# Kernel tuning notes

Measured on AMD Instinct MI355X. Metric: run time of the kernel, lower is better.

The kernel has to match this reference:

```python
import jax, jax.numpy as jnp
import numpy as np

N = 100000      # nodes
E = 3200000     # edges
IN_DIM = 128
HID = 128
OUT_DIM = 1
LAYERS = 8
ALPHA = 0.1
THETA = 0.5


def setup_inputs() -> dict:
    key = jax.random.key(0)
    ks = jax.random.split(key, 8)
    x = jax.random.normal(ks[0], (N, IN_DIM), dtype=jnp.float32)
    edge_index = jax.random.randint(ks[1], (2, E), 0, N, dtype=jnp.int64)
    edge_weight = jax.random.uniform(ks[2], (E,), dtype=jnp.float32)  # unused by original forward path
    W_in = jax.random.normal(ks[3], (IN_DIM, HID), dtype=jnp.float32) * 0.05
    b_in = jnp.zeros((HID,), dtype=jnp.float32)
    W_gcn = jax.random.normal(ks[4], (LAYERS, HID, HID), dtype=jnp.float32) * 0.05
    W_out = jax.random.normal(ks[5], (HID, OUT_DIM), dtype=jnp.float32) * 0.05
    b_out = jnp.zeros((OUT_DIM,), dtype=jnp.float32)
    return {"x": x, "edge_weight": edge_weight, "W_in": W_in, "b_in": b_in,
            "W_gcn": W_gcn, "W_out": W_out, "b_out": b_out, "edge_index": edge_index}


def _gcn_norm(edge_index, dtype):
    # add self loops (fill value 1), symmetric normalization deg^-1/2 A deg^-1/2
    sl = jnp.arange(N, dtype=edge_index.dtype)
    row = jnp.concatenate([edge_index[0], sl])
    col = jnp.concatenate([edge_index[1], sl])
    w = jnp.ones(row.shape[0], dtype=dtype)
    deg = jax.ops.segment_sum(w, col, num_segments=N)
    dinv = jnp.where(deg > 0, jax.lax.rsqrt(deg), 0.0)
    norm = dinv[row] * dinv[col]
    return row, col, norm


def reference(x, edge_weight, W_in, b_in, W_gcn, W_out, b_out, edge_index):
    row, col, norm = _gcn_norm(edge_index, x.dtype)
    h = x @ W_in + b_in            # initial_proj
    h0 = h                          # residual x0
    for i in range(LAYERS):
        # dropout is identity in eval mode
        msg = h[row] * norm[:, None]                       # gather + scale [E+N, HID]
        agg = jax.ops.segment_sum(msg, col, num_segments=N)
        s = (1.0 - ALPHA) * agg + ALPHA * h0               # identity-mapped residual
        beta = float(np.log(THETA / (i + 1) + 1.0))
        h = (1.0 - beta) * s + beta * (s @ W_gcn[i])       # GCNII weight mix
        h = jax.nn.relu(h)
    return h @ W_out + b_out
```

## Files before the change

### kernel.cpp

```cpp
#include <hip/hip_runtime.h>
#include <hip/hip_bf16.h>
#include <math.h>

#define N_NODES 100000
#define N_EDGES 3200000
#define HID 128
#define LAYERS 8
#define ALPHA 0.1f
#define THETA 0.5f

#define SCAN_TILE 1024
#define NB_SCAN ((N_NODES + SCAN_TILE - 1) / SCAN_TILE)

typedef unsigned int uint;
typedef unsigned short ushort;
typedef __attribute__((ext_vector_type(8))) short short8;
typedef __attribute__((ext_vector_type(4))) float f32x4;

__device__ inline float bf_lo(uint p) { return __uint_as_float(p << 16); }
__device__ inline float bf_hi(uint p) { return __uint_as_float(p & 0xffff0000u); }
__device__ inline uint bf_pack(float x, float y) {
    uint ux = __float_as_uint(x), uy = __float_as_uint(y);
    uint rx = (ux + 0x7fffu + ((ux >> 16) & 1u)) >> 16;
    uint ry = (uy + 0x7fffu + ((uy >> 16) & 1u)) >> 16;
    return rx | (ry << 16);
}
__device__ inline ushort bfr(float x) {
    uint u = __float_as_uint(x);
    return (ushort)((u + 0x7fffu + ((u >> 16) & 1u)) >> 16);
}
__device__ inline float bff(ushort s) { return __uint_as_float(((uint)s) << 16); }

__global__ __launch_bounds__(256) void k_count(const int* __restrict__ col,
                                               int* __restrict__ cnt) {
    int e = blockIdx.x * 256 + threadIdx.x;
    if (e < N_EDGES) atomicAdd(&cnt[col[e]], 1);
}

__global__ __launch_bounds__(256) void k_dinv(const int* __restrict__ cnt,
                                              float* __restrict__ dinv) {
    int n = blockIdx.x * 256 + threadIdx.x;
    if (n < N_NODES) dinv[n] = rsqrtf((float)(cnt[n] + 1));
}

__global__ __launch_bounds__(256) void k_scan1(const int* __restrict__ cnt,
                                               int* __restrict__ indptr,
                                               int* __restrict__ bsum) {
    __shared__ int lds[256];
    int t = threadIdx.x;
    int base = blockIdx.x * SCAN_TILE + t * 4;
    int v[4];
    int s = 0;
#pragma unroll
    for (int j = 0; j < 4; ++j) {
        v[j] = (base + j < N_NODES) ? cnt[base + j] : 0;
        s += v[j];
    }
    lds[t] = s;
    __syncthreads();
    for (int off = 1; off < 256; off <<= 1) {
        int u = (t >= off) ? lds[t - off] : 0;
        __syncthreads();
        lds[t] += u;
        __syncthreads();
    }
    int run = lds[t] - s;
#pragma unroll
    for (int j = 0; j < 4; ++j) {
        if (base + j < N_NODES) indptr[base + j] = run;
        run += v[j];
    }
    if (t == 255) bsum[blockIdx.x] = lds[255];
}

__global__ __launch_bounds__(256) void k_scan2(const int* __restrict__ bsum,
                                               int* __restrict__ boff) {
    __shared__ int lds[256];
    int t = threadIdx.x;
    int v = (t < NB_SCAN) ? bsum[t] : 0;
    lds[t] = v;
    __syncthreads();
    for (int off = 1; off < 256; off <<= 1) {
        int u = (t >= off) ? lds[t - off] : 0;
        __syncthreads();
        lds[t] += u;
        __syncthreads();
    }
    boff[t] = lds[t] - v;
}

__global__ __launch_bounds__(256) void k_scan3(int* __restrict__ indptr,
                                               const int* __restrict__ boff) {
    int base = blockIdx.x * SCAN_TILE + threadIdx.x * 4;
    int add = boff[blockIdx.x];
#pragma unroll
    for (int j = 0; j < 4; ++j) {
        if (base + j < N_NODES) indptr[base + j] += add;
    }
    if (blockIdx.x == 0 && threadIdx.x == 0) indptr[N_NODES] = N_EDGES;
}

__global__ __launch_bounds__(256) void k_fill(const int* __restrict__ rowi,
                                              const int* __restrict__ coli,
                                              const float* __restrict__ dinv,
                                              const int* __restrict__ indptr,
                                              int* __restrict__ cursor,
                                              int2* __restrict__ csr) {
    int e = blockIdx.x * 256 + threadIdx.x;
    if (e >= N_EDGES) return;
    int r = rowi[e];
    int c = coli[e];
    int p = indptr[c] + atomicAdd(&cursor[c], 1);
    csr[p] = make_int2(r, __float_as_int(dinv[r] * dinv[c]));
}

__global__ __launch_bounds__(256) void k_wprep(const float* __restrict__ Wg,
                                               ushort* __restrict__ Wt) {
    int l = blockIdx.x;
    const float* W = Wg + (size_t)l * HID * HID;
    ushort* T = Wt + (size_t)l * HID * HID;
    int t = threadIdx.x;
#pragma unroll
    for (int i = 0; i < 16; ++i) {
        int idx = t + 256 * i;
        int k = idx >> 5;
        int c4 = idx & 31;
        float4 v = *(const float4*)(W + (size_t)k * HID + c4 * 4);
        T[(c4 * 4 + 0) * HID + k] = bfr(v.x);
        T[(c4 * 4 + 1) * HID + k] = bfr(v.y);
        T[(c4 * 4 + 2) * HID + k] = bfr(v.z);
        T[(c4 * 4 + 3) * HID + k] = bfr(v.w);
    }
}

__global__ __launch_bounds__(256) void k_spmm(const uint* __restrict__ h,
                                              const uint* __restrict__ h0,
                                              const float* __restrict__ dinv,
                                              const int* __restrict__ indptr,
                                              const int2* __restrict__ csr,
                                              uint* __restrict__ s_out) {
    int node = blockIdx.x * 4 + (threadIdx.x >> 6);
    if (node >= N_NODES) return;
    int lane = threadIdx.x & 63;
    int beg = indptr[node];
    int end = indptr[node + 1];
    float di = dinv[node];
    uint hs = h[node * 64 + lane];
    uint h0v = h0[node * 64 + lane];
    float ax[8], ay[8];
#pragma unroll
    for (int j = 0; j < 8; ++j) { ax[j] = 0.f; ay[j] = 0.f; }
    int e = beg;
    for (; e + 16 <= end; e += 16) {
        int2 rr[16];
#pragma unroll
        for (int j = 0; j < 16; ++j) rr[j] = csr[e + j];
        uint p[16];
#pragma unroll
        for (int j = 0; j < 16; ++j) p[j] = h[rr[j].x * 64 + lane];
#pragma unroll
        for (int j = 0; j < 16; ++j) {
            float w = __int_as_float(rr[j].y);
            ax[j & 7] = fmaf(w, bf_lo(p[j]), ax[j & 7]);
            ay[j & 7] = fmaf(w, bf_hi(p[j]), ay[j & 7]);
        }
    }
    for (; e < end; e += 4) {
        int2 rr[4];
        float w[4];
#pragma unroll
        for (int j = 0; j < 4; ++j) {
            int idx = e + j;
            rr[j] = csr[idx < end ? idx : beg];
            w[j] = (idx < end) ? __int_as_float(rr[j].y) : 0.f;
        }
        uint p[4];
#pragma unroll
        for (int j = 0; j < 4; ++j) p[j] = h[rr[j].x * 64 + lane];
#pragma unroll
        for (int j = 0; j < 4; ++j) {
            ax[j] = fmaf(w[j], bf_lo(p[j]), ax[j]);
            ay[j] = fmaf(w[j], bf_hi(p[j]), ay[j]);
        }
    }
    float sum0 = ((ax[0] + ax[1]) + (ax[2] + ax[3])) + ((ax[4] + ax[5]) + (ax[6] + ax[7]));
    float sum1 = ((ay[0] + ay[1]) + (ay[2] + ay[3])) + ((ay[4] + ay[5]) + (ay[6] + ay[7]));
    float selfw = di * di;
    float rx = (1.0f - ALPHA) * fmaf(selfw, bf_lo(hs), sum0) + ALPHA * bf_lo(h0v);
    float ry = (1.0f - ALPHA) * fmaf(selfw, bf_hi(hs), sum1) + ALPHA * bf_hi(h0v);
    s_out[node * 64 + lane] = bf_pack(rx, ry);
}

__global__ __launch_bounds__(256) void k_gemm_in(const float* __restrict__ A,
                                                 const float* __restrict__ W,
                                                 const float* __restrict__ bias,
                                                 uint* __restrict__ out0,
                                                 uint* __restrict__ out1) {
    __shared__ float sT[32 * 64];
    __shared__ float Ws[32 * 128];
    int t = threadIdx.x;
    int tr = t & 15;
    int tc = t >> 4;
    int rowBase = blockIdx.x * 64;
    float acc[4][8] = {};

    for (int ko = 0; ko < HID; ko += 32) {
#pragma unroll
        for (int pass = 0; pass < 2; ++pass) {
            int lin = t + 256 * pass;
            int r = lin >> 3;
            int kq = lin & 7;
            int ar = rowBase + r;
            if (ar >= N_NODES) ar = N_NODES - 1;
            float4 v = *(const float4*)(A + (size_t)ar * HID + ko + 4 * kq);
            sT[(4 * kq + 0) * 64 + r] = v.x;
            sT[(4 * kq + 1) * 64 + r] = v.y;
            sT[(4 * kq + 2) * 64 + r] = v.z;
            sT[(4 * kq + 3) * 64 + r] = v.w;
        }
#pragma unroll
        for (int pass = 0; pass < 4; ++pass) {
            int lin = t + 256 * pass;
            int k = lin >> 5;
            int c4 = lin & 31;
            *(float4*)&Ws[k * 128 + 4 * c4] =
                *(const float4*)(W + (size_t)(ko + k) * HID + 4 * c4);
        }
        __syncthreads();
#pragma unroll
        for (int k = 0; k < 32; ++k) {
            float4 a = *(const float4*)&sT[k * 64 + 4 * tr];
            float4 w0 = *(const float4*)&Ws[k * 128 + 8 * tc];
            float4 w1 = *(const float4*)&Ws[k * 128 + 8 * tc + 4];
            float av[4] = {a.x, a.y, a.z, a.w};
            float wv[8] = {w0.x, w0.y, w0.z, w0.w, w1.x, w1.y, w1.z, w1.w};
#pragma unroll
            for (int i = 0; i < 4; ++i)
#pragma unroll
                for (int j = 0; j < 8; ++j)
                    acc[i][j] = fmaf(av[i], wv[j], acc[i][j]);
        }
        __syncthreads();
    }

    int c0 = 8 * tc;
    float bb[8];
#pragma unroll
    for (int j = 0; j < 8; ++j) bb[j] = bias[c0 + j];
#pragma unroll
    for (int i = 0; i < 4; ++i) {
        int r = rowBase + 4 * tr + i;
        if (r >= N_NODES) break;
        float v[8];
#pragma unroll
        for (int j = 0; j < 8; ++j) v[j] = acc[i][j] + bb[j];
        uint4 o;
        o.x = bf_pack(v[0], v[1]);
        o.y = bf_pack(v[2], v[3]);
        o.z = bf_pack(v[4], v[5]);
        o.w = bf_pack(v[6], v[7]);
        *(uint4*)(out0 + (size_t)r * 64 + c0 / 2) = o;
        *(uint4*)(out1 + (size_t)r * 64 + c0 / 2) = o;
    }
}

#define SAS 136

__global__ __launch_bounds__(256) void k_gemm_layer(const uint* __restrict__ A,
                                                    const ushort* __restrict__ Wt,
                                                    uint* __restrict__ out0,
                                                    float beta) {
    __shared__ ushort sA[64 * SAS];
    __shared__ ushort sW[128 * SAS];
    int t = threadIdx.x;
    int lane = t & 63;
    int wv = t >> 6;
    int rowBase = blockIdx.x * 64;

#pragma unroll
    for (int i = 0; i < 4; ++i) {
        int idx = t + 256 * i;
        int r = idx >> 4;
        int q = idx & 15;
        int ar = rowBase + r;
        if (ar >= N_NODES) ar = N_NODES - 1;
        uint4 v = *(const uint4*)(A + (size_t)ar * 64 + q * 4);
        *(uint4*)((uint*)(sA + r * SAS) + q * 4) = v;
    }
#pragma unroll
    for (int i = 0; i < 8; ++i) {
        int idx = t + 256 * i;
        int r = idx >> 4;
        int q = idx & 15;
        uint4 v = *(const uint4*)((const uint*)(Wt + (size_t)r * HID) + q * 4);
        *(uint4*)((uint*)(sW + r * SAS) + q * 4) = v;
    }
    __syncthreads();

    int fr = lane & 15;
    int fq = lane >> 4;
    f32x4 acc[4][2] = {};
#pragma unroll
    for (int kc = 0; kc < 4; ++kc) {
        int kof = kc * 32 + fq * 8;
        short8 b0 = *(const short8*)(sW + (wv * 32 + fr) * SAS + kof);
        short8 b1 = *(const short8*)(sW + (wv * 32 + 16 + fr) * SAS + kof);
#pragma unroll
        for (int tm = 0; tm < 4; ++tm) {
            short8 a = *(const short8*)(sA + (tm * 16 + fr) * SAS + kof);
            acc[tm][0] = __builtin_amdgcn_mfma_f32_16x16x32_bf16(a, b0, acc[tm][0], 0, 0, 0);
            acc[tm][1] = __builtin_amdgcn_mfma_f32_16x16x32_bf16(a, b1, acc[tm][1], 0, 0, 0);
        }
    }
    __syncthreads();

    ushort* pack = sW;
    float ob = 1.0f - beta;
#pragma unroll
    for (int tm = 0; tm < 4; ++tm)
#pragma unroll
        for (int tn = 0; tn < 2; ++tn)
#pragma unroll
            for (int r = 0; r < 4; ++r) {
                int row = tm * 16 + fq * 4 + r;
                int col = wv * 32 + tn * 16 + fr;
                float sv = bff(sA[row * SAS + col]);
                float val = fmaxf(fmaf(ob, sv, beta * acc[tm][tn][r]), 0.f);
                pack[row * 128 + col] = bfr(val);
            }
    __syncthreads();
#pragma unroll
    for (int i = 0; i < 4; ++i) {
        int idx = t + 256 * i;
        int r = idx >> 4;
        int q = idx & 15;
        int ar = rowBase + r;
        if (ar < N_NODES)
            *(uint4*)(out0 + (size_t)ar * 64 + q * 4) =
                *(const uint4*)((const uint*)(pack + r * 128) + q * 4);
    }
}

__global__ __launch_bounds__(256) void k_out(const uint* __restrict__ h,
                                             const float* __restrict__ W_out,
                                             const float* __restrict__ b_out,
                                             float* __restrict__ out) {
    int node = blockIdx.x * 4 + (threadIdx.x >> 6);
    if (node >= N_NODES) return;
    int lane = threadIdx.x & 63;
    uint p = h[node * 64 + lane];
    float2 wv = *(const float2*)(W_out + lane * 2);
    float pr = bf_lo(p) * wv.x + bf_hi(p) * wv.y;
#pragma unroll
    for (int off = 32; off > 0; off >>= 1) pr += __shfl_down(pr, off);
    if (lane == 0) out[node] = pr + b_out[0];
}

extern "C" void kernel_launch(void* const* d_in, const int* in_sizes, int n_in,
                              void* d_out, int out_size, void* d_ws, size_t ws_size,
                              hipStream_t stream) {
    const float* x     = (const float*)d_in[0];
    const float* W_in  = (const float*)d_in[2];
    const float* b_in  = (const float*)d_in[3];
    const float* W_gcn = (const float*)d_in[4];
    const float* W_out = (const float*)d_in[5];
    const float* b_out = (const float*)d_in[6];
    const int*   ei    = (const int*)d_in[7];
    const int* rowi = ei;
    const int* coli = ei + N_EDGES;
    float* out = (float*)d_out;

    char* ws = (char*)d_ws;
    auto alloc = [&](size_t bytes) -> char* {
        char* p = ws;
        ws += (bytes + 255) & ~(size_t)255;
        return p;
    };
    int*    cnt     = (int*)   alloc((size_t)N_NODES * 4);
    float*  dinv    = (float*) alloc((size_t)N_NODES * 4);
    int*    indptr  = (int*)   alloc((size_t)(N_NODES + 1) * 4);
    int*    cursor  = (int*)   alloc((size_t)N_NODES * 4);
    int*    bsum    = (int*)   alloc(1024 * 4);
    int*    boff    = (int*)   alloc(1024 * 4);
    int2*   csr     = (int2*)  alloc((size_t)N_EDGES * 8);
    ushort* Wt      = (ushort*)alloc((size_t)LAYERS * HID * HID * 2);
    uint*   hA      = (uint*)  alloc((size_t)N_NODES * 64 * 4);
    uint*   hB      = (uint*)  alloc((size_t)N_NODES * 64 * 4);
    uint*   h0      = (uint*)  alloc((size_t)N_NODES * 64 * 4);

    hipMemsetAsync(cnt, 0, (size_t)N_NODES * 4, stream);
    hipMemsetAsync(cursor, 0, (size_t)N_NODES * 4, stream);

    k_count<<<(N_EDGES + 255) / 256, 256, 0, stream>>>(coli, cnt);
    k_dinv<<<(N_NODES + 255) / 256, 256, 0, stream>>>(cnt, dinv);
    k_scan1<<<NB_SCAN, 256, 0, stream>>>(cnt, indptr, bsum);
    k_scan2<<<1, 256, 0, stream>>>(bsum, boff);
    k_scan3<<<NB_SCAN, 256, 0, stream>>>(indptr, boff);
    k_fill<<<(N_EDGES + 255) / 256, 256, 0, stream>>>(rowi, coli, dinv, indptr,
                                                      cursor, csr);
    k_wprep<<<LAYERS, 256, 0, stream>>>(W_gcn, Wt);

    int gemm_blocks = (N_NODES + 63) / 64;
    k_gemm_in<<<gemm_blocks, 256, 0, stream>>>(x, W_in, b_in, h0, hA);

    for (int l = 0; l < LAYERS; ++l) {
        k_spmm<<<(N_NODES + 3) / 4, 256, 0, stream>>>(hA, h0, dinv, indptr,
                                                      csr, hB);
        float beta = logf(THETA / (float)(l + 1) + 1.0f);
        k_gemm_layer<<<gemm_blocks, 256, 0, stream>>>(
            hB, Wt + (size_t)l * HID * HID, hA, beta);
    }
    k_out<<<(N_NODES + 3) / 4, 256, 0, stream>>>(hA, W_out, b_out, out);
}
```

Measured before the change: 1.525 ms.

## Build CSR via two-level bucket sort with LDS-local atomics

Replaces the global-atomic count, three-pass scan and scatter fill with a bucketed construction. Edges are first binned into 391 buckets of 256 destination nodes using LDS atomics, with one global atomic per bucket per block. Per-bucket kernels then compute degrees, dinv and indptr, and scatter CSR entries using LDS cursors. This aims to cut global atomic contention and scattered accesses, at the cost of an extra pass over the edges and a fixed bucket capacity (10240) that reuses the hB buffer and could overflow for skewed degree distributions.

```diff
diff --git a/kernel.cpp b/kernel.cpp
--- a/kernel.cpp
+++ b/kernel.cpp
@@ -9,8 +9,10 @@
 #define ALPHA 0.1f
 #define THETA 0.5f
 
-#define SCAN_TILE 1024
-#define NB_SCAN ((N_NODES + SCAN_TILE - 1) / SCAN_TILE)
+#define NBKT 391
+#define BKT_STRIDE 10240
+#define EPT 16
+#define CHUNK 4096
 
 typedef unsigned int uint;
 typedef unsigned short ushort;
@@ -31,87 +33,118 @@
 }
 __device__ inline float bff(ushort s) { return __uint_as_float(((uint)s) << 16); }
 
-__global__ __launch_bounds__(256) void k_count(const int* __restrict__ col,
-                                               int* __restrict__ cnt) {
-    int e = blockIdx.x * 256 + threadIdx.x;
-    if (e < N_EDGES) atomicAdd(&cnt[col[e]], 1);
-}
-
-__global__ __launch_bounds__(256) void k_dinv(const int* __restrict__ cnt,
-                                              float* __restrict__ dinv) {
-    int n = blockIdx.x * 256 + threadIdx.x;
-    if (n < N_NODES) dinv[n] = rsqrtf((float)(cnt[n] + 1));
-}
-
-__global__ __launch_bounds__(256) void k_scan1(const int* __restrict__ cnt,
-                                               int* __restrict__ indptr,
-                                               int* __restrict__ bsum) {
-    __shared__ int lds[256];
-    int t = threadIdx.x;
-    int base = blockIdx.x * SCAN_TILE + t * 4;
-    int v[4];
-    int s = 0;
-#pragma unroll
-    for (int j = 0; j < 4; ++j) {
-        v[j] = (base + j < N_NODES) ? cnt[base + j] : 0;
-        s += v[j];
-    }
-    lds[t] = s;
+__global__ __launch_bounds__(256) void k_bucket(const int* __restrict__ rowi,
+                                                const int* __restrict__ coli,
+                                                uint* __restrict__ eb,
+                                                int* __restrict__ gcnt) {
+    __shared__ int bcnt[NBKT];
+    __shared__ int gbase[NBKT];
+    int t = threadIdx.x;
+    for (int i = t; i < NBKT; i += 256) bcnt[i] = 0;
+    __syncthreads();
+
+    int e0 = blockIdx.x * CHUNK;
+    int bk[EPT];
+    int rk[EPT];
+    uint rec[EPT];
+#pragma unroll
+    for (int j = 0; j < EPT; ++j) {
+        int e = e0 + j * 256 + t;
+        if (e < N_EDGES) {
+            int r = rowi[e];
+            int c = coli[e];
+            bk[j] = c >> 8;
+            rec[j] = ((uint)r << 8) | (uint)(c & 255);
+            rk[j] = atomicAdd(&bcnt[bk[j]], 1);
+        } else {
+            bk[j] = -1;
+        }
+    }
+    __syncthreads();
+    for (int i = t; i < NBKT; i += 256) {
+        int n = bcnt[i];
+        gbase[i] = n ? atomicAdd(&gcnt[i], n) : 0;
+    }
+    __syncthreads();
+#pragma unroll
+    for (int j = 0; j < EPT; ++j) {
+        if (bk[j] >= 0)
+            eb[(size_t)bk[j] * BKT_STRIDE + gbase[bk[j]] + rk[j]] = rec[j];
+    }
+}
+
+__global__ __launch_bounds__(512) void k_bscan(const int* __restrict__ gcnt,
+                                               int* __restrict__ bbase) {
+    __shared__ int lds[512];
+    int t = threadIdx.x;
+    int v = (t < NBKT) ? gcnt[t] : 0;
+    lds[t] = v;
+    __syncthreads();
+    for (int off = 1; off < 512; off <<= 1) {
+        int u = (t >= off) ? lds[t - off] : 0;
+        __syncthreads();
+        lds[t] += u;
+        __syncthreads();
+    }
+    if (t < NBKT) bbase[t] = lds[t] - v;
+}
+
+__global__ __launch_bounds__(256) void k_node_ipt(const uint* __restrict__ eb,
+                                                  const int* __restrict__ gcnt,
+                                                  const int* __restrict__ bbase,
+                                                  float* __restrict__ dinv,
+                                                  int* __restrict__ indptr) {
+    __shared__ int ncnt[256];
+    __shared__ int sc[256];
+    int b = blockIdx.x;
+    int t = threadIdx.x;
+    ncnt[t] = 0;
+    __syncthreads();
+    int ne = gcnt[b];
+    const uint* ebp = eb + (size_t)b * BKT_STRIDE;
+    for (int i = t; i < ne; i += 256) atomicAdd(&ncnt[ebp[i] & 255], 1);
+    __syncthreads();
+    int v = ncnt[t];
+    sc[t] = v;
     __syncthreads();
     for (int off = 1; off < 256; off <<= 1) {
-        int u = (t >= off) ? lds[t - off] : 0;
-        __syncthreads();
-        lds[t] += u;
-        __syncthreads();
-    }
-    int run = lds[t] - s;
-#pragma unroll
-    for (int j = 0; j < 4; ++j) {
-        if (base + j < N_NODES) indptr[base + j] = run;
-        run += v[j];
-    }
-    if (t == 255) bsum[blockIdx.x] = lds[255];
-}
-
-__global__ __launch_bounds__(256) void k_scan2(const int* __restrict__ bsum,
-                                               int* __restrict__ boff) {
-    __shared__ int lds[256];
-    int t = threadIdx.x;
-    int v = (t < NB_SCAN) ? bsum[t] : 0;
-    lds[t] = v;
-    __syncthreads();
-    for (int off = 1; off < 256; off <<= 1) {
-        int u = (t >= off) ? lds[t - off] : 0;
-        __syncthreads();
-        lds[t] += u;
-        __syncthreads();
-    }
-    boff[t] = lds[t] - v;
-}
-
-__global__ __launch_bounds__(256) void k_scan3(int* __restrict__ indptr,
-                                               const int* __restrict__ boff) {
-    int base = blockIdx.x * SCAN_TILE + threadIdx.x * 4;
-    int add = boff[blockIdx.x];
-#pragma unroll
-    for (int j = 0; j < 4; ++j) {
-        if (base + j < N_NODES) indptr[base + j] += add;
-    }
-    if (blockIdx.x == 0 && threadIdx.x == 0) indptr[N_NODES] = N_EDGES;
-}
-
-__global__ __launch_bounds__(256) void k_fill(const int* __restrict__ rowi,
-                                              const int* __restrict__ coli,
-                                              const float* __restrict__ dinv,
-                                              const int* __restrict__ indptr,
-                                              int* __restrict__ cursor,
-                                              int2* __restrict__ csr) {
-    int e = blockIdx.x * 256 + threadIdx.x;
-    if (e >= N_EDGES) return;
-    int r = rowi[e];
-    int c = coli[e];
-    int p = indptr[c] + atomicAdd(&cursor[c], 1);
-    csr[p] = make_int2(r, __float_as_int(dinv[r] * dinv[c]));
+        int u = (t >= off) ? sc[t - off] : 0;
+        __syncthreads();
+        sc[t] += u;
+        __syncthreads();
+    }
+    int node = b * 256 + t;
+    if (node < N_NODES) {
+        dinv[node] = rsqrtf((float)(v + 1));
+        indptr[node] = bbase[b] + (sc[t] - v);
+    }
+    if (b == NBKT - 1 && t == 255) indptr[N_NODES] = N_EDGES;
+}
+
+__global__ __launch_bounds__(256) void k_fill2(const uint* __restrict__ eb,
+                                               const int* __restrict__ gcnt,
+                                               const float* __restrict__ dinv,
+                                               const int* __restrict__ indptr,
+                                               int2* __restrict__ csr) {
+    __shared__ float sdv[256];
+    __shared__ int scur[256];
+    __shared__ int sipt[256];
+    int b = blockIdx.x;
+    int t = threadIdx.x;
+    int node = b * 256 + t;
+    sdv[t] = (node < N_NODES) ? dinv[node] : 0.f;
+    sipt[t] = (node < N_NODES) ? indptr[node] : 0;
+    scur[t] = 0;
+    __syncthreads();
+    int ne = gcnt[b];
+    const uint* ebp = eb + (size_t)b * BKT_STRIDE;
+    for (int i = t; i < ne; i += 256) {
+        uint rec = ebp[i];
+        int lc = rec & 255;
+        int r = (int)(rec >> 8);
+        int pos = sipt[lc] + atomicAdd(&scur[lc], 1);
+        csr[pos] = make_int2(r, __float_as_int(dinv[r] * sdv[lc]));
+    }
 }
 
 __global__ __launch_bounds__(256) void k_wprep(const float* __restrict__ Wg,
@@ -376,28 +409,23 @@
         ws += (bytes + 255) & ~(size_t)255;
         return p;
     };
-    int*    cnt     = (int*)   alloc((size_t)N_NODES * 4);
     float*  dinv    = (float*) alloc((size_t)N_NODES * 4);
     int*    indptr  = (int*)   alloc((size_t)(N_NODES + 1) * 4);
-    int*    cursor  = (int*)   alloc((size_t)N_NODES * 4);
-    int*    bsum    = (int*)   alloc(1024 * 4);
-    int*    boff    = (int*)   alloc(1024 * 4);
+    int*    gcnt    = (int*)   alloc(2048 * 4);
+    int*    bbase   = (int*)   alloc(2048 * 4);
     int2*   csr     = (int2*)  alloc((size_t)N_EDGES * 8);
     ushort* Wt      = (ushort*)alloc((size_t)LAYERS * HID * HID * 2);
     uint*   hA      = (uint*)  alloc((size_t)N_NODES * 64 * 4);
     uint*   hB      = (uint*)  alloc((size_t)N_NODES * 64 * 4);
     uint*   h0      = (uint*)  alloc((size_t)N_NODES * 64 * 4);
-
-    hipMemsetAsync(cnt, 0, (size_t)N_NODES * 4, stream);
-    hipMemsetAsync(cursor, 0, (size_t)N_NODES * 4, stream);
-
-    k_count<<<(N_EDGES + 255) / 256, 256, 0, stream>>>(coli, cnt);
-    k_dinv<<<(N_NODES + 255) / 256, 256, 0, stream>>>(cnt, dinv);
-    k_scan1<<<NB_SCAN, 256, 0, stream>>>(cnt, indptr, bsum);
-    k_scan2<<<1, 256, 0, stream>>>(bsum, boff);
-    k_scan3<<<NB_SCAN, 256, 0, stream>>>(indptr, boff);
-    k_fill<<<(N_EDGES + 255) / 256, 256, 0, stream>>>(rowi, coli, dinv, indptr,
-                                                      cursor, csr);
+    uint*   eb      = hB;
+
+    hipMemsetAsync(gcnt, 0, (size_t)NBKT * 4, stream);
+
+    k_bucket<<<(N_EDGES + CHUNK - 1) / CHUNK, 256, 0, stream>>>(rowi, coli, eb, gcnt);
+    k_bscan<<<1, 512, 0, stream>>>(gcnt, bbase);
+    k_node_ipt<<<NBKT, 256, 0, stream>>>(eb, gcnt, bbase, dinv, indptr);
+    k_fill2<<<NBKT, 256, 0, stream>>>(eb, gcnt, dinv, indptr, csr);
     k_wprep<<<LAYERS, 256, 0, stream>>>(W_gcn, Wt);
 
     int gemm_blocks = (N_NODES + 63) / 64;
```

Measured after the change: 1.307 ms. 14.3% less time.
